# Kernel optimization log

Measured on AMD Instinct MI355X. Metric: run time of the kernel, lower is better.

Reference implementation:

```python
import jax, jax.numpy as jnp
import numpy as np

NUM_TOKENS = 32000
DIM = 1024
DEPTH = 4
HEADS = 16
DIM_HEAD = 64
FF_MULT = 4
DH_FF = int(DIM * FF_MULT * 2 / 3)  # 2730
B, N = 2, 2048
ROPE_THETA = 10000.0


def setup_inputs() -> dict:
    key = jax.random.key(0)
    ks = jax.random.split(key, 8)
    s = 0.02
    return {
        "tokens": jax.random.randint(ks[0], (B, N), 0, NUM_TOKENS),
        "token_emb": jax.random.normal(ks[1], (NUM_TOKENS, DIM)) * s,
        "attn_norm_w": jnp.ones((DEPTH, DIM)),
        "wqkv": jax.random.normal(ks[2], (DEPTH, DIM, 3 * HEADS * DIM_HEAD)) * s,
        "wo": jax.random.normal(ks[3], (DEPTH, HEADS * DIM_HEAD, DIM)) * s,
        "ff_norm_w": jnp.ones((DEPTH, DIM)),
        "ff_w1": jax.random.normal(ks[4], (DEPTH, DIM, 2 * DH_FF)) * s,
        "ff_b1": jnp.zeros((DEPTH, 2 * DH_FF)),
        "ff_w2": jax.random.normal(ks[5], (DEPTH, DH_FF, DIM)) * s,
        "ff_b2": jnp.zeros((DEPTH, DIM)),
        "final_norm_w": jnp.ones((DIM,)),
        "logits_w": jax.random.normal(ks[6], (DIM, NUM_TOKENS)) * s,
        "logits_b": jnp.zeros((NUM_TOKENS,)),
    }


def rmsnorm(x, w):
    eps = jnp.finfo(x.dtype).eps  # torch RMSNorm default eps
    var = jnp.mean(jnp.square(x), axis=-1, keepdims=True)
    return x * jax.lax.rsqrt(var + eps) * w


def rotate_half(x):
    x1, x2 = jnp.split(x, 2, axis=-1)
    return jnp.concatenate((-x2, x1), axis=-1)


def apply_rope(pos, t):
    return t * jnp.cos(pos) + rotate_half(t) * jnp.sin(pos)


def reference(tokens, token_emb, attn_norm_w, wqkv, wo, ff_norm_w,
              ff_w1, ff_b1, ff_w2, ff_b2, final_norm_w, logits_w, logits_b):
    b, n = tokens.shape
    x = token_emb[tokens]  # [b, n, dim]

    # rotary embedding table [n, dim_head]
    inv_freq = ROPE_THETA ** (-(jnp.arange(0, DIM_HEAD, 2, dtype=jnp.float32) / DIM_HEAD))
    freqs = jnp.arange(n, dtype=jnp.float32)[:, None] * inv_freq[None, :]
    pos = jnp.concatenate((freqs, freqs), axis=-1)

    scale = DIM_HEAD ** -0.5
    causal = jnp.triu(jnp.ones((n, n), dtype=bool), 1)

    for l in range(DEPTH):
        # --- attention ---
        h = rmsnorm(x, attn_norm_w[l])
        qkv = jnp.einsum('bnd,de->bne', h, wqkv[l])
        qkv = qkv.reshape(b, n, 3, HEADS, DIM_HEAD)
        qkv = jnp.transpose(qkv, (2, 0, 3, 1, 4))  # [3, b, h, n, d]
        q, k, v = qkv[0], qkv[1], qkv[2]
        q = apply_rope(pos, q)
        k = apply_rope(pos, k)
        q = q * scale
        sim = jnp.einsum('bhid,bhjd->bhij', q, k)
        sim = jnp.where(causal, -jnp.finfo(sim.dtype).max, sim)
        attn = jax.nn.softmax(sim, axis=-1)
        out = jnp.einsum('bhij,bhjd->bhid', attn, v)
        out = jnp.transpose(out, (0, 2, 1, 3)).reshape(b, n, HEADS * DIM_HEAD)
        x = jnp.einsum('bne,ed->bnd', out, wo[l]) + x

        # --- GEGLU feedforward ---
        h = rmsnorm(x, ff_norm_w[l])
        u = jnp.einsum('bnd,de->bne', h, ff_w1[l]) + ff_b1[l]
        u1, gate = jnp.split(u, 2, axis=-1)
        g = jax.nn.gelu(gate, approximate=False) * u1
        x = jnp.einsum('bne,ed->bnd', g, ff_w2[l]) + ff_b2[l] + x

    embed = rmsnorm(x, final_norm_w)
    logits = jnp.einsum('bnd,dv->bnv', embed, logits_w) + logits_b
    return logits
```

## Files before the change

kernel.cpp:

```cpp
#include <hip/hip_runtime.h>
#include <math.h>
#include <stdint.h>


using short8v = __attribute__((ext_vector_type(8))) short;
using f32x4   = __attribute__((ext_vector_type(4))) float;

__device__ __forceinline__ float b2f(short s) {
    union { unsigned u; float f; } v; v.u = ((unsigned)(unsigned short)s) << 16; return v.f;
}
__device__ __forceinline__ short f2b(float f) {
    union { float f; unsigned u; } v; v.f = f;
    unsigned r = v.u + 0x7FFFu + ((v.u >> 16) & 1u);
    return (short)(r >> 16);
}

__device__ __forceinline__ void mfma_n(f32x4& d, short8v a, short8v b) {
    asm("v_mfma_f32_16x16x32_bf16 %0, %1, %2, %0" : "+v"(d) : "v"(a), "v"(b));
}
__device__ __forceinline__ void mfma_f(f32x4& d, short8v a, short8v b) {
    asm("s_nop 1\n\tv_mfma_f32_16x16x32_bf16 %0, %1, %2, %0" : "+v"(d) : "v"(a), "v"(b));
}
#define MFMA_FENCE() do { __builtin_amdgcn_sched_barrier(0); \
    asm volatile("s_nop 7\n\ts_nop 7"); \
    __builtin_amdgcn_sched_barrier(0); } while (0)

__device__ __forceinline__ void gload16(const void* g, void* l) {
    __builtin_amdgcn_global_load_lds(
        (const __attribute__((address_space(1))) unsigned int*)(uintptr_t)g,
        (__attribute__((address_space(3))) unsigned int*)(uintptr_t)l,
        16, 0, 0);
}

#define BARX() do { asm volatile("" ::: "memory"); \
    __builtin_amdgcn_s_barrier(); asm volatile("" ::: "memory"); } while (0)
#define VMN(n) asm volatile("s_waitcnt vmcnt(" #n ")" ::: "memory")
#define LGKM0() do { asm volatile("s_waitcnt lgkmcnt(0)" ::: "memory"); \
    __builtin_amdgcn_sched_barrier(0); } while (0)

__global__ void rope_table_k(float* __restrict__ ct, float* __restrict__ st) {
    int i = blockIdx.x * 256 + threadIdx.x;
    int n = i >> 5, j = i & 31;
    float freq = expf(-(float)j * (9.210340371976184f / 32.f));
    float a = (float)n * freq;
    ct[i] = cosf(a);
    st[i] = sinf(a);
}

__global__ void embed_k(const int* __restrict__ tok, const float* __restrict__ emb,
                        float* __restrict__ x) {
    int row = blockIdx.x;
    int tk = tok[row];
    const float4* src = (const float4*)(emb + (size_t)tk * 1024);
    float4* dst = (float4*)(x + (size_t)row * 1024);
    dst[threadIdx.x] = src[threadIdx.x];
}

__global__ void wconv_k(const float* __restrict__ W, short* __restrict__ T,
                        int K, int N, int Kpad,
                        size_t w_lstride, size_t t_lstride) {
    W += blockIdx.z * w_lstride;
    T += blockIdx.z * t_lstride;
    int n0 = blockIdx.x * 32, k0 = blockIdx.y * 32;
    __shared__ float tile[32][33];
    int t = threadIdx.x;
    int kk = t >> 3, ns = (t & 7) * 4;
    float4 v = make_float4(0.f, 0.f, 0.f, 0.f);
    int gk = k0 + kk;
    if (gk < K) {
        if (n0 + ns + 3 < N) {
            v = *(const float4*)(W + (size_t)gk * N + n0 + ns);
        } else {
            float tmp[4] = {0.f, 0.f, 0.f, 0.f};
            #pragma unroll
            for (int j = 0; j < 4; ++j)
                if (n0 + ns + j < N) tmp[j] = W[(size_t)gk * N + n0 + ns + j];
            v = make_float4(tmp[0], tmp[1], tmp[2], tmp[3]);
        }
    }
    tile[kk][ns + 0] = v.x; tile[kk][ns + 1] = v.y;
    tile[kk][ns + 2] = v.z; tile[kk][ns + 3] = v.w;
    __syncthreads();
    int nn = t >> 3, ks = (t & 7) * 4;
    short o[4];
    #pragma unroll
    for (int j = 0; j < 4; ++j) o[j] = f2b(tile[ks + j][nn]);
    *(int2*)(T + (size_t)(n0 + nn) * Kpad + k0 + ks) = *(int2*)o;
}

__global__ void rmsnorm_k(const float* __restrict__ x, const float* __restrict__ wt,
                          short* __restrict__ out) {
    int row = blockIdx.x;
    int t = threadIdx.x;
    const float* xr = x + (size_t)row * 1024;
    float4 v = ((const float4*)xr)[t];
    float ss = v.x * v.x + v.y * v.y + v.z * v.z + v.w * v.w;
    #pragma unroll
    for (int off = 32; off > 0; off >>= 1) ss += __shfl_down(ss, off, 64);
    __shared__ float red[4];
    if ((t & 63) == 0) red[t >> 6] = ss;
    __syncthreads();
    float tot = red[0] + red[1] + red[2] + red[3];
    float inv = rsqrtf(tot * (1.f / 1024.f) + 1.1920929e-7f);
    float4 wv = ((const float4*)wt)[t];
    int2 pk;
    pk.x = (int)(unsigned short)f2b(v.x * inv * wv.x) |
           ((int)(unsigned short)f2b(v.y * inv * wv.y) << 16);
    pk.y = (int)(unsigned short)f2b(v.z * inv * wv.z) |
           ((int)(unsigned short)f2b(v.w * inv * wv.w) << 16);
    *(int2*)(out + (size_t)row * 1024 + t * 4) = pk;
}

__global__ void geglu_k(const short* __restrict__ u, short* __restrict__ gbuf) {
    int r = blockIdx.x;
    int c = blockIdx.y * 256 + threadIdx.x;
    if (c >= 2752) return;
    float v = 0.f;
    if (c < 2730) {
        float u1 = b2f(u[(size_t)r * 5460 + c]);
        float gt = b2f(u[(size_t)r * 5460 + 2730 + c]);
        v = 0.5f * gt * (1.f + erff(gt * 0.7071067811865475f)) * u1;
    }
    gbuf[(size_t)r * 2752 + c] = f2b(v);
}

template <bool BIAS, bool RES, bool OUTBF16>
__global__ __launch_bounds__(256, 4) void gemm2h(
    const short* __restrict__ A, const short* __restrict__ Bt,
    const float* __restrict__ bias, const float* __restrict__ res,
    void* __restrict__ outp, int N, int lda, int ldb, int ksteps) {
    __shared__ __align__(16) short As[64 * 32];
    __shared__ __align__(16) short Bs[128 * 32];
    const int t = threadIdx.x;
    const int lane = t & 63;
    const int w = t >> 6, wm = w >> 1, wn = w & 1;
    const int c = lane & 15, g = lane >> 4;

    const int nwg = (int)gridDim.x;
    const int cpx = nwg >> 3;
    const int wg = ((int)blockIdx.x & 7) * cpx + ((int)blockIdx.x >> 3);
    const int m0 = (wg & 63) << 6;
    const int n0 = (wg >> 6) << 7;

    const int srow = w * 16 + (lane >> 2);
    const int sseg = (lane & 3) * 8;
    const short* ga0 = A  + (size_t)(m0 + srow) * lda + sseg;
    const short* gb0 = Bt + (size_t)(n0 + w * 32 + (lane >> 2)) * ldb + sseg;
    const short* gb1 = Bt + (size_t)(n0 + w * 32 + 16 + (lane >> 2)) * ldb + sseg;
    short* la0 = &As[w * 512];
    short* lb0 = &Bs[(w * 2 + 0) * 512];
    short* lb1 = &Bs[(w * 2 + 1) * 512];

    f32x4 acc[2][4] = {};

    for (int kt = 0; kt < ksteps; ++kt) {
        const int k0 = kt << 5;
        __syncthreads();
        gload16(ga0 + k0, la0);
        gload16(gb0 + k0, lb0);
        gload16(gb1 + k0, lb1);
        __syncthreads();
        short8v af[2], bf[4];
        #pragma unroll
        for (int mi = 0; mi < 2; ++mi)
            af[mi] = *(const short8v*)&As[(wm * 32 + mi * 16 + c) * 32 + g * 8];
        #pragma unroll
        for (int ni = 0; ni < 4; ++ni)
            bf[ni] = *(const short8v*)&Bs[(wn * 64 + ni * 16 + c) * 32 + g * 8];
        #pragma unroll
        for (int mi = 0; mi < 2; ++mi)
            #pragma unroll
            for (int ni = 0; ni < 4; ++ni)
                mfma_n(acc[mi][ni], af[mi], bf[ni]);
    }
    MFMA_FENCE();
    #pragma unroll
    for (int mi = 0; mi < 2; ++mi) {
        #pragma unroll
        for (int ni = 0; ni < 4; ++ni) {
            int col = n0 + wn * 64 + ni * 16 + c;
            if (col < N) {
                float bv = BIAS ? bias[col] : 0.f;
                #pragma unroll
                for (int i = 0; i < 4; ++i) {
                    int row = m0 + wm * 32 + mi * 16 + g * 4 + i;
                    size_t off = (size_t)row * N + col;
                    float v = acc[mi][ni][i] + bv;
                    if (RES) v += res[off];
                    if (OUTBF16) ((short*)outp)[off] = f2b(v);
                    else         ((float*)outp)[off] = v;
                }
            }
        }
    }
}

template <bool BIAS, bool RES, bool OUTBF16, bool ROPE>
__global__ __launch_bounds__(512, 1) void gemm3(
    const short* __restrict__ A, const short* __restrict__ Bt,
    const float* __restrict__ bias, const float* __restrict__ res,
    void* __restrict__ outp, int N, int lda, int ldb, int nrowsB, int KT,
    const float* __restrict__ ct, const float* __restrict__ st,
    short* __restrict__ vtb) {
    __shared__ __align__(16) short L[49152];
    const int t = threadIdx.x;
    const int lane = t & 63;
    const int w = t >> 6;
    const int wm = w >> 2, wn = w & 3;
    const int c = lane & 15, g = lane >> 4;

    const int nwg = (int)gridDim.x, cpx = nwg >> 3;
    const int wg = ((int)blockIdx.x & 7) * cpx + ((int)blockIdx.x >> 3);
    const int m0 = (wg & 31) << 7;
    const int n0 = (wg >> 5) << 8;

    const int rS = t >> 3, sS = t & 7;
    const int sSw = (sS ^ (rS & 7)) << 3;
    size_t aoffh[2], broff[2][2];
    #pragma unroll
    for (int h = 0; h < 2; ++h)
        aoffh[h] = (size_t)(m0 + h * 64 + rS) * lda + sSw;
    #pragma unroll
    for (int h = 0; h < 2; ++h)
        #pragma unroll
        for (int i = 0; i < 2; ++i) {
            int brow = n0 + h * 128 + rS + i * 64;
            if (brow > nrowsB - 1) brow = nrowsB - 1;
            broff[h][i] = (size_t)brow * ldb + sSw;
        }
    short* ldsA[2][2];
    short* ldsB[2][2];
    #pragma unroll
    for (int p = 0; p < 2; ++p)
        #pragma unroll
        for (int h = 0; h < 2; ++h) {
            ldsA[p][h] = &L[(p * 2 + h) * 4096 + w * 512];
            ldsB[p][h] = &L[16384 + (p * 2 + h) * 8192 + w * 512];
        }

    const int cb0 = ((g * 8) ^ ((c & 7) * 8));
    const int vbA0 = wm * 4096 + c * 64 + cb0;
    const int vbA1 = vbA0 ^ 32;
    const int vbB0 = 16384 + (wn >> 1) * 8192 + (wn & 1) * 4096 + c * 64 + cb0;
    const int vbB1 = vbB0 ^ 32;

    #define STA3(p, h, kt) gload16(A + aoffh[h] + (kt) * 64, ldsA[p][h])
    #define STB3(p, h, kt) do { \
        gload16(Bt + broff[h][0] + (kt) * 64, ldsB[p][h]); \
        gload16(Bt + broff[h][1] + (kt) * 64, ldsB[p][h] + 4096); } while (0)
    #define LDA3(p, mi, ks) (*(const short8v*)&L[(p) * 8192 + (mi) * 1024 + ((ks) ? vbA1 : vbA0)])
    #define LDB3(p, ni, ks) (*(const short8v*)&L[(p) * 16384 + (ni) * 1024 + ((ks) ? vbB1 : vbB0)])
    #define MFMA8(MLO, NLO, BV) do { \
        _Pragma("unroll") for (int ks_ = 0; ks_ < 2; ++ks_) \
        _Pragma("unroll") for (int mi_ = 0; mi_ < 2; ++mi_) \
        _Pragma("unroll") for (int ni_ = 0; ni_ < 2; ++ni_) \
            mfma_n(acc[(MLO) + mi_][(NLO) + ni_], av[(MLO) + mi_][ks_], BV[(NLO) + ni_][ks_]); \
        } while (0)

    f32x4 acc[4][4] = {};
    short8v av[4][2], bc[4][2], bn[4][2];

    STB3(0, 1, 0); STB3(0, 0, 0); STA3(0, 0, 0); STA3(0, 1, 0);
    STB3(1, 1, 1); STB3(1, 0, 1); STA3(1, 0, 1); STA3(1, 1, 1);
    VMN(6);
    BARX();
    #pragma unroll
    for (int ni = 0; ni < 4; ++ni)
        #pragma unroll
        for (int ks = 0; ks < 2; ++ks)
            bc[ni][ks] = LDB3(0, ni, ks);
    LGKM0();
    BARX();
    asm volatile("s_nop 7\n\ts_nop 7");

    for (int KB = 0; KB < KT; KB += 2) {
        const bool st1 = (KB + 2 < KT);
        const bool st2 = (KB + 3 < KT);
        #pragma unroll
        for (int mi = 0; mi < 2; ++mi)
            #pragma unroll
            for (int ks = 0; ks < 2; ++ks) av[mi][ks] = LDA3(0, mi, ks);
        if (st1) STB3(0, 1, KB + 2);
        BARX();
        __builtin_amdgcn_s_setprio(1); MFMA8(0, 0, bc); __builtin_amdgcn_s_setprio(0);
        BARX();
        #pragma unroll
        for (int mi = 2; mi < 4; ++mi)
            #pragma unroll
            for (int ks = 0; ks < 2; ++ks) av[mi][ks] = LDA3(0, mi, ks);
        if (st1) { STB3(0, 0, KB + 2); VMN(6); } else { VMN(2); }
        BARX();
        __builtin_amdgcn_s_setprio(1); MFMA8(2, 0, bc); __builtin_amdgcn_s_setprio(0);
        BARX();
        #pragma unroll
        for (int ni = 0; ni < 2; ++ni)
            #pragma unroll
            for (int ks = 0; ks < 2; ++ks) bn[ni][ks] = LDB3(1, ni, ks);
        if (st1) STA3(0, 0, KB + 2);
        BARX();
        __builtin_amdgcn_s_setprio(1); MFMA8(0, 2, bc); __builtin_amdgcn_s_setprio(0);
        BARX();
        #pragma unroll
        for (int ni = 2; ni < 4; ++ni)
            #pragma unroll
            for (int ks = 0; ks < 2; ++ks) bn[ni][ks] = LDB3(1, ni, ks);
        if (st1) { STA3(0, 1, KB + 2); VMN(6); } else { VMN(0); }
        BARX();
        __builtin_amdgcn_s_setprio(1); MFMA8(2, 2, bc); __builtin_amdgcn_s_setprio(0);
        BARX();
        #pragma unroll
        for (int mi = 0; mi < 2; ++mi)
            #pragma unroll
            for (int ks = 0; ks < 2; ++ks) av[mi][ks] = LDA3(1, mi, ks);
        if (st2) STB3(1, 1, KB + 3);
        BARX();
        __builtin_amdgcn_s_setprio(1); MFMA8(0, 0, bn); __builtin_amdgcn_s_setprio(0);
        BARX();
        #pragma unroll
        for (int mi = 2; mi < 4; ++mi)
            #pragma unroll
            for (int ks = 0; ks < 2; ++ks) av[mi][ks] = LDA3(1, mi, ks);
        if (st2) STB3(1, 0, KB + 3);
        if (st1) VMN(6);
        BARX();
        __builtin_amdgcn_s_setprio(1); MFMA8(2, 0, bn); __builtin_amdgcn_s_setprio(0);
        BARX();
        if (st1) {
            #pragma unroll
            for (int ni = 0; ni < 2; ++ni)
                #pragma unroll
                for (int ks = 0; ks < 2; ++ks) bc[ni][ks] = LDB3(0, ni, ks);
        }
        if (st2) STA3(1, 0, KB + 3);
        BARX();
        __builtin_amdgcn_s_setprio(1); MFMA8(0, 2, bn); __builtin_amdgcn_s_setprio(0);
        BARX();
        if (st1) {
            #pragma unroll
            for (int ni = 2; ni < 4; ++ni)
                #pragma unroll
                for (int ks = 0; ks < 2; ++ks) bc[ni][ks] = LDB3(0, ni, ks);
        }
        if (st2) STA3(1, 1, KB + 3);
        if (st1) VMN(6);
        BARX();
        __builtin_amdgcn_s_setprio(1); MFMA8(2, 2, bn); __builtin_amdgcn_s_setprio(0);
        BARX();
    }

    MFMA_FENCE();

    if (ROPE) {
        const int colbase = n0 + wn * 64;
        const int sec = colbase >> 10;
        if (sec < 2) {
            const float sc = (sec == 0) ? 0.125f : 1.0f;
            #pragma unroll
            for (int mi = 0; mi < 4; ++mi)
                #pragma unroll
                for (int ni = 0; ni < 2; ++ni) {
                    const int col = colbase + ni * 16 + c;
                    const int jj = ni * 16 + c;
                    #pragma unroll
                    for (int i = 0; i < 4; ++i) {
                        int row = m0 + wm * 64 + mi * 16 + g * 4 + i;
                        int n = row & 2047;
                        float cv = ct[n * 32 + jj], sv = st[n * 32 + jj];
                        float a = acc[mi][ni][i], b = acc[mi][ni + 2][i];
                        ((short*)outp)[(size_t)row * N + col]      = f2b((a * cv - b * sv) * sc);
                        ((short*)outp)[(size_t)row * N + col + 32] = f2b((b * cv + a * sv) * sc);
                    }
                }
        } else {
            const int h64 = (colbase - 2048) >> 6;
            #pragma unroll
            for (int mi = 0; mi < 4; ++mi) {
                const int r0 = m0 + wm * 64 + mi * 16 + g * 4;
                const int bb = r0 >> 11, nn = r0 & 2047;
                #pragma unroll
                for (int ni = 0; ni < 4; ++ni) {
                    const int d = ni * 16 + c;
                    short s4[4];
                    #pragma unroll
                    for (int i = 0; i < 4; ++i) s4[i] = f2b(acc[mi][ni][i]);
                    *(int2*)(vtb + (size_t)((bb * 16 + h64) * 64 + d) * 2048 + nn) =
                        *(int2*)s4;
                }
            }
        }
        return;
    }

    #pragma unroll
    for (int mi = 0; mi < 4; ++mi) {
        #pragma unroll
        for (int ni = 0; ni < 4; ++ni) {
            int col = n0 + wn * 64 + ni * 16 + c;
            if (col < N) {
                float bv = BIAS ? bias[col] : 0.f;
                #pragma unroll
                for (int i = 0; i < 4; ++i) {
                    int row = m0 + wm * 64 + mi * 16 + g * 4 + i;
                    size_t off = (size_t)row * N + col;
                    float v = acc[mi][ni][i] + bv;
                    if (RES) v += res[off];
                    if (OUTBF16) ((short*)outp)[off] = f2b(v);
                    else         ((float*)outp)[off] = v;
                }
            }
        }
    }
    #undef STA3
    #undef STB3
    #undef LDA3
    #undef LDB3
    #undef MFMA8
}

template <bool BIAS, bool RES, bool OUTBF16>
__global__ __launch_bounds__(512, 2) void gemm4(
    const short* __restrict__ A, const short* __restrict__ Bt,
    const float* __restrict__ bias, const float* __restrict__ res,
    void* __restrict__ outp, int N, int lda, int ldb, int nrowsB, int KT) {
    __shared__ __align__(16) short L[65536];
    const int t = threadIdx.x;
    const int lane = t & 63;
    const int w = t >> 6;
    const int wm = w >> 2, wn = w & 3;
    const int c = lane & 15, g = lane >> 4;

    const int nwg = (int)gridDim.x, cpx = nwg >> 3;
    const int wg = ((int)blockIdx.x & 7) * cpx + ((int)blockIdx.x >> 3);
    const int m0 = (wg & 15) << 8;
    const int n0 = (wg >> 4) << 8;

    const int sub0 = t & 63;
    const int seg0 = sub0 >> 4, r0 = sub0 & 15;
    const int slab0 = t >> 6, slab1 = slab0 + 8;
    const size_t aoff0 = (size_t)(m0 + slab0 * 16 + r0) * lda + seg0 * 8;
    const size_t aoff1 = (size_t)(m0 + slab1 * 16 + r0) * lda + seg0 * 8;
    int br0 = n0 + slab0 * 16 + r0; if (br0 > nrowsB - 1) br0 = nrowsB - 1;
    int br1 = n0 + slab1 * 16 + r0; if (br1 > nrowsB - 1) br1 = nrowsB - 1;
    const size_t boff0 = (size_t)br0 * ldb + seg0 * 8;
    const size_t boff1 = (size_t)br1 * ldb + seg0 * 8;

    char* Lb = (char*)L;
    const int rb = g * 256 + c * 16;

    #define STA4(p, kh, kt) do { \
        gload16(A + aoff0 + (kt) * 64 + (kh) * 32, Lb + ((p)*2+(kh))*16384 + w*1024); \
        gload16(A + aoff1 + (kt) * 64 + (kh) * 32, Lb + ((p)*2+(kh))*16384 + 8192 + w*1024); } while (0)
    #define STB4(p, kh, kt) do { \
        gload16(Bt + boff0 + (kt) * 64 + (kh) * 32, Lb + 65536 + ((p)*2+(kh))*16384 + w*1024); \
        gload16(Bt + boff1 + (kt) * 64 + (kh) * 32, Lb + 65536 + ((p)*2+(kh))*16384 + 8192 + w*1024); } while (0)
    #define LDA4(p, ks, mi) (*(const short8v*)(Lb + ((p)*2+(ks))*16384 + (wm*8+(mi))*1024 + rb))
    #define LDB4(p, ks, ni) (*(const short8v*)(Lb + 65536 + ((p)*2+(ks))*16384 + (wn*4+(ni))*1024 + rb))
    #define MFMAQ(MB) do { \
        _Pragma("unroll") for (int mi_ = 0; mi_ < 4; ++mi_) \
        _Pragma("unroll") for (int ni_ = 0; ni_ < 4; ++ni_) \
            mfma_n(acc[(MB) + mi_][ni_], av[mi_], bv[ni_]); } while (0)

    f32x4 acc[8][4] = {};
    short8v av[4], bv[4];

    STA4(0, 0, 0); STB4(0, 0, 0); STA4(0, 1, 0); STB4(0, 1, 0);
    VMN(4);
    BARX();
    asm volatile("s_nop 7\n\ts_nop 7");

    #define TILE4(p, pn, tc, stg2) do { \
        _Pragma("unroll") for (int mi = 0; mi < 4; ++mi) av[mi] = LDA4(p, 0, mi); \
        _Pragma("unroll") for (int ni = 0; ni < 4; ++ni) bv[ni] = LDB4(p, 0, ni); \
        if (stg2) STA4(pn, 0, (tc) + 1); \
        BARX(); \
        __builtin_amdgcn_s_setprio(1); MFMAQ(0); __builtin_amdgcn_s_setprio(0); \
        BARX(); \
        _Pragma("unroll") for (int mi = 0; mi < 4; ++mi) av[mi] = LDA4(p, 0, mi + 4); \
        if (stg2) { STB4(pn, 0, (tc) + 1); VMN(4); } else { VMN(0); } \
        BARX(); \
        __builtin_amdgcn_s_setprio(1); MFMAQ(4); __builtin_amdgcn_s_setprio(0); \
        BARX(); \
        _Pragma("unroll") for (int mi = 0; mi < 4; ++mi) av[mi] = LDA4(p, 1, mi); \
        _Pragma("unroll") for (int ni = 0; ni < 4; ++ni) bv[ni] = LDB4(p, 1, ni); \
        if (stg2) STA4(pn, 1, (tc) + 1); \
        BARX(); \
        __builtin_amdgcn_s_setprio(1); MFMAQ(0); __builtin_amdgcn_s_setprio(0); \
        BARX(); \
        _Pragma("unroll") for (int mi = 0; mi < 4; ++mi) av[mi] = LDA4(p, 1, mi + 4); \
        if (stg2) { STB4(pn, 1, (tc) + 1); VMN(4); } \
        BARX(); \
        __builtin_amdgcn_s_setprio(1); MFMAQ(4); __builtin_amdgcn_s_setprio(0); \
        BARX(); \
    } while (0)

    for (int kt = 0; kt < KT; kt += 2) {
        TILE4(0, 1, kt, true);
        TILE4(1, 0, kt + 1, (kt + 2 < KT));
    }
    #undef TILE4

    MFMA_FENCE();
    #pragma unroll
    for (int mi = 0; mi < 8; ++mi) {
        #pragma unroll
        for (int ni = 0; ni < 4; ++ni) {
            int col = n0 + wn * 64 + ni * 16 + c;
            if (col < N) {
                float bvv = BIAS ? bias[col] : 0.f;
                #pragma unroll
                for (int i = 0; i < 4; ++i) {
                    int row = m0 + wm * 128 + mi * 16 + g * 4 + i;
                    size_t off = (size_t)row * N + col;
                    float v = acc[mi][ni][i] + bvv;
                    if (RES) v += res[off];
                    if (OUTBF16) ((short*)outp)[off] = f2b(v);
                    else         ((float*)outp)[off] = v;
                }
            }
        }
    }
    #undef STA4
    #undef STB4
    #undef LDA4
    #undef LDB4
    #undef MFMAQ
}

__global__ __launch_bounds__(256, 2) void attn_fwd(
    const short* __restrict__ qkv, const short* __restrict__ vt,
    short* __restrict__ o) {
    const int qt = blockIdx.x, bh = blockIdx.y;
    const int b = bh >> 4, h = bh & 15;
    const int t = threadIdx.x, lane = t & 63, w = t >> 6;
    const int c = lane & 15, g = lane >> 4;
    __shared__ __align__(16) short Ks[128 * 72];
    __shared__ __align__(16) short Vs[64 * 136];
    __shared__ __align__(16) short Ps[128 * 136];

    #pragma unroll
    for (int i = 0; i < 4; ++i) {
        int idx = t + i * 256, r = idx >> 3, seg = idx & 7;
        *(int4*)&Ps[r * 136 + seg * 8] =
            *(const int4*)(qkv + (size_t)(b * 2048 + qt * 128 + r) * 3072 + h * 64 + seg * 8);
    }
    __syncthreads();
    short8v qf[2][2];
    #pragma unroll
    for (int mi = 0; mi < 2; ++mi)
        #pragma unroll
        for (int kk = 0; kk < 2; ++kk)
            qf[mi][kk] = *(const short8v*)&Ps[(w * 32 + mi * 16 + c) * 136 + kk * 32 + g * 8];

    f32x4 oacc[2][4] = {};
    float mrow[2][4], lrow[2][4];
    #pragma unroll
    for (int mi = 0; mi < 2; ++mi)
        #pragma unroll
        for (int i = 0; i < 4; ++i) { mrow[mi][i] = -3.0e38f; lrow[mi][i] = 0.f; }

    for (int jt = 0; jt <= qt; ++jt) {
        __syncthreads();
        #pragma unroll
        for (int i = 0; i < 4; ++i) {
            int idx = t + i * 256, r = idx >> 3, seg = idx & 7;
            *(int4*)&Ks[r * 72 + seg * 8] =
                *(const int4*)(qkv + (size_t)(b * 2048 + jt * 128 + r) * 3072
                               + 1024 + h * 64 + seg * 8);
        }
        #pragma unroll
        for (int i = 0; i < 4; ++i) {
            int idx = t + i * 256, d = idx >> 4, seg = idx & 15;
            *(int4*)&Vs[d * 136 + seg * 8] =
                *(const int4*)(vt + (size_t)(bh * 64 + d) * 2048 + jt * 128 + seg * 8);
        }
        __syncthreads();
        f32x4 sacc[2][8] = {};
        #pragma unroll
        for (int kk = 0; kk < 2; ++kk) {
            short8v kf[8];
            #pragma unroll
            for (int ni = 0; ni < 8; ++ni)
                kf[ni] = *(const short8v*)&Ks[(ni * 16 + c) * 72 + kk * 32 + g * 8];
            #pragma unroll
            for (int mi = 0; mi < 2; ++mi)
                #pragma unroll
                for (int ni = 0; ni < 8; ++ni) {
                    if (kk == 0) mfma_f(sacc[mi][ni], qf[mi][kk], kf[ni]);
                    else         mfma_n(sacc[mi][ni], qf[mi][kk], kf[ni]);
                }
        }
        MFMA_FENCE();
        if (jt == qt) {
            #pragma unroll
            for (int mi = 0; mi < 2; ++mi)
                #pragma unroll
                for (int ni = 0; ni < 8; ++ni)
                    #pragma unroll
                    for (int i = 0; i < 4; ++i) {
                        int qrow = w * 32 + mi * 16 + g * 4 + i;
                        int kcol = ni * 16 + c;
                        if (kcol > qrow) sacc[mi][ni][i] = -3.0e38f;
                    }
        }
        #pragma unroll
        for (int mi = 0; mi < 2; ++mi) {
            #pragma unroll
            for (int i = 0; i < 4; ++i) {
                float mx = sacc[mi][0][i];
                #pragma unroll
                for (int ni = 1; ni < 8; ++ni) mx = fmaxf(mx, sacc[mi][ni][i]);
                #pragma unroll
                for (int off = 1; off < 16; off <<= 1) mx = fmaxf(mx, __shfl_xor(mx, off, 64));
                float mnew = fmaxf(mrow[mi][i], mx);
                float alpha = __expf(mrow[mi][i] - mnew);
                mrow[mi][i] = mnew;
                float ls = 0.f;
                #pragma unroll
                for (int ni = 0; ni < 8; ++ni) {
                    float p = __expf(sacc[mi][ni][i] - mnew);
                    sacc[mi][ni][i] = p;
                    ls += p;
                }
                #pragma unroll
                for (int off = 1; off < 16; off <<= 1) ls += __shfl_xor(ls, off, 64);
                lrow[mi][i] = lrow[mi][i] * alpha + ls;
                #pragma unroll
                for (int df = 0; df < 4; ++df) oacc[mi][df][i] *= alpha;
            }
        }
        #pragma unroll
        for (int mi = 0; mi < 2; ++mi)
            #pragma unroll
            for (int ni = 0; ni < 8; ++ni)
                #pragma unroll
                for (int i = 0; i < 4; ++i)
                    Ps[(w * 32 + mi * 16 + g * 4 + i) * 136 + ni * 16 + c] =
                        f2b(sacc[mi][ni][i]);
        #pragma unroll
        for (int kk = 0; kk < 4; ++kk) {
            short8v pf[2], vf[4];
            #pragma unroll
            for (int mi = 0; mi < 2; ++mi)
                pf[mi] = *(const short8v*)&Ps[(w * 32 + mi * 16 + c) * 136 + kk * 32 + g * 8];
            #pragma unroll
            for (int df = 0; df < 4; ++df)
                vf[df] = *(const short8v*)&Vs[(df * 16 + c) * 136 + kk * 32 + g * 8];
            #pragma unroll
            for (int mi = 0; mi < 2; ++mi)
                #pragma unroll
                for (int df = 0; df < 4; ++df) {
                    if (kk == 0) mfma_f(oacc[mi][df], pf[mi], vf[df]);
                    else         mfma_n(oacc[mi][df], pf[mi], vf[df]);
                }
        }
    }
    MFMA_FENCE();
    #pragma unroll
    for (int mi = 0; mi < 2; ++mi)
        #pragma unroll
        for (int df = 0; df < 4; ++df)
            #pragma unroll
            for (int i = 0; i < 4; ++i) {
                int qrow = qt * 128 + w * 32 + mi * 16 + g * 4 + i;
                float v = oacc[mi][df][i] / lrow[mi][i];
                o[(size_t)(b * 2048 + qrow) * 1024 + h * 64 + df * 16 + c] = f2b(v);
            }
}

extern "C" void kernel_launch(void* const* d_in, const int* in_sizes, int n_in,
                              void* d_out, int out_size, void* d_ws, size_t ws_size,
                              hipStream_t stream) {
    (void)in_sizes; (void)n_in; (void)out_size; (void)ws_size;
    const int*   tokens = (const int*)d_in[0];
    const float* temb   = (const float*)d_in[1];
    const float* anw    = (const float*)d_in[2];
    const float* wqkv   = (const float*)d_in[3];
    const float* wo     = (const float*)d_in[4];
    const float* fnw    = (const float*)d_in[5];
    const float* fw1    = (const float*)d_in[6];
    const float* fb1    = (const float*)d_in[7];
    const float* fw2    = (const float*)d_in[8];
    const float* fb2    = (const float*)d_in[9];
    const float* finw   = (const float*)d_in[10];
    const float* lw     = (const float*)d_in[11];
    const float* lb     = (const float*)d_in[12];

    char* ws = (char*)d_ws;
    float* x    = (float*)(ws + 0);
    short* hb   = (short*)(ws + 16777216);
    short* qkv  = (short*)(ws + 25165824);
    short* ao   = (short*)(ws + 50331648);
    short* ub   = (short*)(ws + 58720256);
    short* gb   = (short*)(ws + 103448576);
    short* vtb  = (short*)(ws + 125992960);
    float* ct   = (float*)(ws + 134381568);
    float* st   = (float*)(ws + 134643712);
    short* qkvT = (short*)(ws + 134905856);
    short* woT  = (short*)(ws + 160071680);
    short* fw1T = (short*)(ws + 168460288);
    short* fw2T = (short*)(ws + 213549056);
    short* logT = (short*)(ws + 236093440);

    rope_table_k<<<256, 256, 0, stream>>>(ct, st);
    embed_k<<<4096, 256, 0, stream>>>(tokens, temb, x);

    wconv_k<<<dim3(96, 32, 4), 256, 0, stream>>>(
        wqkv, qkvT, 1024, 3072, 1024, (size_t)1024 * 3072, (size_t)3072 * 1024);
    wconv_k<<<dim3(32, 32, 4), 256, 0, stream>>>(
        wo, woT, 1024, 1024, 1024, (size_t)1024 * 1024, (size_t)1024 * 1024);
    wconv_k<<<dim3(172, 32, 4), 256, 0, stream>>>(
        fw1, fw1T, 1024, 5460, 1024, (size_t)1024 * 5460, (size_t)5504 * 1024);
    wconv_k<<<dim3(32, 86, 4), 256, 0, stream>>>(
        fw2, fw2T, 2730, 1024, 2752, (size_t)2730 * 1024, (size_t)1024 * 2752);
    wconv_k<<<dim3(1000, 32, 1), 256, 0, stream>>>(
        lw, logT, 1024, 32000, 1024, 0, 0);

    for (int l = 0; l < 4; ++l) {
        rmsnorm_k<<<4096, 256, 0, stream>>>(x, anw + l * 1024, hb);
        gemm3<false, false, true, true><<<32 * 12, 512, 0, stream>>>(
            hb, qkvT + (size_t)l * 3072 * 1024, nullptr, nullptr, qkv,
            3072, 1024, 1024, 3072, 16, ct, st, vtb);
        attn_fwd<<<dim3(16, 32), 256, 0, stream>>>(qkv, vtb, ao);
        gemm2h<false, true, false><<<512, 256, 0, stream>>>(
            ao, woT + (size_t)l * 1024 * 1024, nullptr, x, x, 1024, 1024, 1024, 32);
        rmsnorm_k<<<4096, 256, 0, stream>>>(x, fnw + l * 1024, hb);
        gemm3<true, false, true, false><<<32 * 22, 512, 0, stream>>>(
            hb, fw1T + (size_t)l * 5504 * 1024, fb1 + l * 5460, nullptr, ub,
            5460, 1024, 1024, 5504, 16, nullptr, nullptr, nullptr);
        geglu_k<<<dim3(4096, 11), 256, 0, stream>>>(ub, gb);
        gemm2h<true, true, false><<<512, 256, 0, stream>>>(
            gb, fw2T + (size_t)l * 1024 * 2752, fb2 + l * 1024, x, x, 1024, 2752, 2752, 86);
    }
    rmsnorm_k<<<4096, 256, 0, stream>>>(x, finw, hb);
    gemm4<true, false, false><<<2000, 512, 0, stream>>>(
        hb, logT, lb, nullptr, d_out, 32000, 1024, 1024, 32000, 16);
}
```

Baseline: 1.899 ms.

## Prefetch next K/V tile into registers in attention and vectorize GEGLU

The attention kernel now issues the global loads for the next K and V tile into registers right after the shared-memory barrier. Those loads overlap with the current tile's MFMA and softmax work instead of stalling at the top of each iteration. The GEGLU kernel processes 8 bf16 elements per thread with 16-byte vector loads and stores, and its grid shrinks to match. The cost is extra registers in attention, which may lower occupancy, and 16-byte loads from addresses that are not 16-byte aligned in the GEGLU input.

```diff
diff --git a/kernel.cpp b/kernel.cpp
--- a/kernel.cpp
+++ b/kernel.cpp
@@ -113,15 +113,32 @@
 
 __global__ void geglu_k(const short* __restrict__ u, short* __restrict__ gbuf) {
     int r = blockIdx.x;
-    int c = blockIdx.y * 256 + threadIdx.x;
-    if (c >= 2752) return;
-    float v = 0.f;
-    if (c < 2730) {
-        float u1 = b2f(u[(size_t)r * 5460 + c]);
-        float gt = b2f(u[(size_t)r * 5460 + 2730 + c]);
-        v = 0.5f * gt * (1.f + erff(gt * 0.7071067811865475f)) * u1;
-    }
-    gbuf[(size_t)r * 2752 + c] = f2b(v);
+    int c8 = blockIdx.y * 256 + threadIdx.x;
+    if (c8 >= 344) return;
+    int c = c8 * 8;
+    short o8[8];
+    if (c + 8 <= 2730) {
+        short8v u1 = *(const short8v*)(u + (size_t)r * 5460 + c);
+        short8v gt = *(const short8v*)(u + (size_t)r * 5460 + 2730 + c);
+        #pragma unroll
+        for (int j = 0; j < 8; ++j) {
+            float g = b2f(gt[j]);
+            o8[j] = f2b(0.5f * g * (1.f + erff(g * 0.7071067811865475f)) * b2f(u1[j]));
+        }
+    } else {
+        #pragma unroll
+        for (int j = 0; j < 8; ++j) {
+            int col = c + j;
+            float v = 0.f;
+            if (col < 2730) {
+                float u1 = b2f(u[(size_t)r * 5460 + col]);
+                float g  = b2f(u[(size_t)r * 5460 + 2730 + col]);
+                v = 0.5f * g * (1.f + erff(g * 0.7071067811865475f)) * u1;
+            }
+            o8[j] = f2b(v);
+        }
+    }
+    *(int4*)(gbuf + (size_t)r * 2752 + c) = *(int4*)o8;
 }
 
 template <bool BIAS, bool RES, bool OUTBF16>
@@ -558,22 +575,34 @@
         #pragma unroll
         for (int i = 0; i < 4; ++i) { mrow[mi][i] = -3.0e38f; lrow[mi][i] = 0.f; }
 
+    int4 kr[4], vr[4];
+    #define LOADKV(JT) do { \
+        _Pragma("unroll") for (int i = 0; i < 4; ++i) { \
+            int idx = t + i * 256, r = idx >> 3, seg = idx & 7; \
+            kr[i] = *(const int4*)(qkv + (size_t)(b * 2048 + (JT) * 128 + r) * 3072 \
+                                   + 1024 + h * 64 + seg * 8); } \
+        _Pragma("unroll") for (int i = 0; i < 4; ++i) { \
+            int idx = t + i * 256, d = idx >> 4, seg = idx & 15; \
+            vr[i] = *(const int4*)(vt + (size_t)(bh * 64 + d) * 2048 + (JT) * 128 + seg * 8); } \
+        } while (0)
+
+    LOADKV(0);
+
     for (int jt = 0; jt <= qt; ++jt) {
         __syncthreads();
         #pragma unroll
         for (int i = 0; i < 4; ++i) {
             int idx = t + i * 256, r = idx >> 3, seg = idx & 7;
-            *(int4*)&Ks[r * 72 + seg * 8] =
-                *(const int4*)(qkv + (size_t)(b * 2048 + jt * 128 + r) * 3072
-                               + 1024 + h * 64 + seg * 8);
+            *(int4*)&Ks[r * 72 + seg * 8] = kr[i];
         }
         #pragma unroll
         for (int i = 0; i < 4; ++i) {
             int idx = t + i * 256, d = idx >> 4, seg = idx & 15;
-            *(int4*)&Vs[d * 136 + seg * 8] =
-                *(const int4*)(vt + (size_t)(bh * 64 + d) * 2048 + jt * 128 + seg * 8);
+            *(int4*)&Vs[d * 136 + seg * 8] = vr[i];
         }
         __syncthreads();
+        if (jt < qt) LOADKV(jt + 1);
+
         f32x4 sacc[2][8] = {};
         #pragma unroll
         for (int kk = 0; kk < 2; ++kk) {
@@ -654,6 +683,7 @@
                 }
         }
     }
+    #undef LOADKV
     MFMA_FENCE();
     #pragma unroll
     for (int mi = 0; mi < 2; ++mi)
@@ -727,7 +757,7 @@
         gemm3<true, false, true, false><<<32 * 22, 512, 0, stream>>>(
             hb, fw1T + (size_t)l * 5504 * 1024, fb1 + l * 5460, nullptr, ub,
             5460, 1024, 1024, 5504, 16, nullptr, nullptr, nullptr);
-        geglu_k<<<dim3(4096, 11), 256, 0, stream>>>(ub, gb);
+        geglu_k<<<dim3(4096, 2), 256, 0, stream>>>(ub, gb);
         gemm2h<true, true, false><<<512, 256, 0, stream>>>(
             gb, fw2T + (size_t)l * 1024 * 2752, fb2 + l * 1024, x, x, 1024, 2752, 2752, 86);
     }
```

Measured after the change: 1.958 ms. 3.1% more time.
